# Kernel tuning notes

Hardware: AMD Instinct MI355X
Metric: run time of the kernel (lower is better)

The kernel has to match this reference:

```python
import jax, jax.numpy as jnp
import numpy as np

TOL = 1e-10
EIG_THRESH = 1e-6
NUM_EIG = 4
LANCZOS_K = 30


def setup_inputs() -> dict:
    key = jax.random.key(0)
    n = 200_000
    m = 3_200_000  # undirected edges, avg degree 16
    k1, k2, k3 = jax.random.split(key, 3)
    src = jax.random.randint(k1, (m,), 0, n, dtype=jnp.int32)
    dst = jax.random.randint(k2, (m,), 0, n, dtype=jnp.int32)
    diag = jnp.arange(n, dtype=jnp.int32)
    # symmetric graph Laplacian L = D - A in COO form: off-diag -1 both directions, diag = degree
    rows = jnp.concatenate([src, dst, diag])
    cols = jnp.concatenate([dst, src, diag])
    deg = jax.ops.segment_sum(jnp.ones(2 * m, jnp.float32),
                              jnp.concatenate([src, dst]), num_segments=n)
    vals = jnp.concatenate([-jnp.ones(2 * m, jnp.float32), deg])
    v0 = jax.random.normal(k3, (n,), jnp.float32)  # plays the role of torch.manual_seed(42) randn
    return {"vals": vals, "v0": v0, "rows": rows, "cols": cols, "n": n}


def reference(vals, v0, rows, cols, n):
    k = min(LANCZOS_K, n - 1)  # = 30 here
    # deterministic start vector: mean-subtract, normalize
    v = v0 - v0.mean()
    v = v / jnp.linalg.norm(v)
    V = jnp.zeros((n, k + 1), jnp.float32).at[:, 0].set(v)
    alphas = jnp.zeros(k, jnp.float32)
    betas = jnp.zeros(k, jnp.float32)

    def matvec(x):  # sparse L @ x via COO gather + segment_sum
        return jax.ops.segment_sum(vals * x[cols], rows, num_segments=n)

    def step(carry, i):
        V, alphas, betas, v_prev, beta_prev, done = carry
        v_cur = jax.lax.dynamic_index_in_dim(V, i, axis=1, keepdims=False)
        w = matvec(v_cur)
        alpha = jnp.dot(v_cur, w)
        w = w - alpha * v_cur - beta_prev * v_prev
        # full reorthogonalization: unset columns of V are zero so projecting on all of V
        # is exactly projecting on V[:, :i+1]
        coeffs = V.T @ w            # (k+1,)
        w = w - V @ coeffs
        w = w - w.mean()
        beta = jnp.linalg.norm(w)
        active = jnp.logical_not(done)
        good = active & (beta >= TOL)
        safe_beta = jnp.maximum(beta, TOL)
        v_next = jnp.where(good, w / safe_beta, 0.0)
        alphas = alphas.at[i].set(jnp.where(active, alpha, 0.0))
        betas = betas.at[i].set(jnp.where(good, beta, 0.0))
        V = V.at[:, i + 1].set(v_next)
        done = done | (beta < TOL)
        return (V, alphas, betas, v_cur, jnp.where(good, beta, 0.0), done), None

    init = (V, alphas, betas, jnp.zeros(n, jnp.float32), jnp.float32(0.0), jnp.array(False))
    (V, alphas, betas, _, _, _), _ = jax.lax.scan(step, init, jnp.arange(k))

    # tridiagonal T; early-break iterations leave zero rows/cols whose zero eigenvalues
    # are filtered by the > 1e-6 threshold, matching the truncated original
    T = jnp.diag(alphas) + jnp.diag(betas[:k - 1], 1) + jnp.diag(betas[:k - 1], -1)
    evals_all, Q = jnp.linalg.eigh(T)  # ascending
    num_valid = jnp.sum(evals_all > EIG_THRESH)
    start = k - num_valid              # valid eigenvalues form the sorted tail (L is PSD)
    pos = jnp.arange(NUM_EIG)
    valid = pos < num_valid
    idx = jnp.clip(start + pos, 0, k - 1)
    sel_evals = jnp.where(valid, evals_all[idx], 0.0)
    Y = Q[:, idx] * valid[None, :].astype(jnp.float32)  # (k, NUM_EIG)
    evecs = V[:, :k] @ Y                                 # (n, NUM_EIG)
    return evecs, sel_evals
```

## Files before the change

kernel.cpp:

```cpp
#include <hip/hip_runtime.h>
#include <math.h>

constexpr int LK = 30;

__device__ __constant__ float SFIX[4] = {1.f, -1.f, -1.f, -1.f};


__device__ __forceinline__ float blockReduceSum(float v) {
    for (int off = 32; off; off >>= 1) v += __shfl_down(v, off);
    __shared__ float s[4];
    int lane = threadIdx.x & 63, wid = threadIdx.x >> 6;
    if (lane == 0) s[wid] = v;
    __syncthreads();
    if (wid == 0) {
        v = (lane < 4) ? s[lane] : 0.f;
        v += __shfl_down(v, 2);
        v += __shfl_down(v, 1);
    }
    return v;
}

__global__ void k_zero_sc(float* __restrict__ sc) {
    sc[threadIdx.x] = 0.f;
    sc[256 + threadIdx.x] = 0.f;
}

__global__ void k_sum(const float* __restrict__ a, int n, float* target) {
    float acc = 0.f;
    for (int r = blockIdx.x * blockDim.x + threadIdx.x; r < n; r += gridDim.x * blockDim.x)
        acc += a[r];
    acc = blockReduceSum(acc);
    if (threadIdx.x == 0) atomicAdd(target, acc);
}

__global__ void k_init_v(const float* __restrict__ v0, float* __restrict__ U, int n,
                         const float* sumv, float* norm_acc, float inv_n) {
    int r = blockIdx.x * 256 + threadIdx.x;
    float m = *sumv * inv_n;
    float t = 0.f;
    if (r < n) { t = v0[r] - m; U[r] = t; }
    float s = blockReduceSum(t * t);
    if (threadIdx.x == 0) atomicAdd(norm_acc, s);
}

__global__ void k_scan1(const float* __restrict__ deg, int* __restrict__ rp,
                        int* __restrict__ bsum, int n) {
    __shared__ int s[256];
    int t = threadIdx.x, g = blockIdx.x * 256 + t;
    int v = (g < n) ? (int)deg[g] : 0;
    s[t] = v;
    __syncthreads();
    for (int off = 1; off < 256; off <<= 1) {
        int add = (t >= off) ? s[t - off] : 0;
        __syncthreads();
        s[t] += add;
        __syncthreads();
    }
    if (g < n) rp[g] = s[t] - v;
    if (t == 255) bsum[blockIdx.x] = s[255];
}

__global__ void k_scan2(int* __restrict__ bsum, int nb) {
    __shared__ int s[1024];
    int t = threadIdx.x;
    int v = (t < nb) ? bsum[t] : 0;
    s[t] = v;
    __syncthreads();
    for (int off = 1; off < 1024; off <<= 1) {
        int add = (t >= off) ? s[t - off] : 0;
        __syncthreads();
        s[t] += add;
        __syncthreads();
    }
    if (t < nb) bsum[t] = s[t] - v;
}

__global__ void k_scan3(int* __restrict__ rp, const int* __restrict__ bsum,
                        int* __restrict__ cursor, int n, int m2) {
    int g = blockIdx.x * 256 + threadIdx.x;
    if (g < n) {
        int v = rp[g] + bsum[blockIdx.x];
        rp[g] = v;
        cursor[g] = v;
    }
    if (g == 0) rp[n] = m2;
}

__global__ void k_fill_part(const int* __restrict__ rows, const int* __restrict__ cols,
                            int* __restrict__ cursor, int* __restrict__ cidx,
                            int m2, int nblk_per_grp) {
    int g = blockIdx.x & 7;
    int bi = blockIdx.x >> 3;
    int stride = nblk_per_grp * 256;
    for (int e = bi * 256 + threadIdx.x; e < m2; e += stride) {
        int r = rows[e];
        if (((r >> 12) & 7) == g) {
            int p = atomicAdd(&cursor[r], 1);
            cidx[p] = cols[e];
        }
    }
}

__global__ void k_matvec(const float* __restrict__ deg, const int* __restrict__ rp,
                         const int* __restrict__ cidx, const float* __restrict__ U,
                         float* __restrict__ Vi, float* __restrict__ w,
                         const float* norm_in, float* __restrict__ coeff,
                         float* __restrict__ alpha_acc, int n) {
    if (blockIdx.x == 0 && threadIdx.x < 33) coeff[threadIdx.x] = 0.f;
    int r = blockIdx.x * 256 + threadIdx.x;
    float part = 0.f;
    if (r < n) {
        float beta = sqrtf(*norm_in);
        float x = U[r] / beta;
        Vi[r] = x;
        int s = rp[r], e = rp[r + 1];
        float su = 0.f;
        int k = s;
        for (; k + 3 < e; k += 4) {
            int c0 = cidx[k], c1 = cidx[k + 1], c2 = cidx[k + 2], c3 = cidx[k + 3];
            float u0 = U[c0], u1 = U[c1], u2 = U[c2], u3 = U[c3];
            su += (u0 + u1) + (u2 + u3);
        }
        for (; k < e; ++k) su += U[cidx[k]];
        float wr = deg[r] * x - su / beta;
        w[r] = wr;
        part = x * wr;
    }
    part = blockReduceSum(part);
    if (threadIdx.x == 0) atomicAdd(alpha_acc, part);
}

__global__ void k_gs1(const float* __restrict__ V, float* __restrict__ w,
                      const float* __restrict__ vcur, const float* __restrict__ vprev,
                      const float* alpha_acc, const float* bprev_sq,
                      float* __restrict__ coeff, int i, int n) {
    __shared__ float slab[32];
    int t = threadIdx.x;
    if (t < 32) slab[t] = 0.f;
    __syncthreads();
    int r = blockIdx.x * 256 + t;
    bool in = (r < n);
    float a = *alpha_acc, b = sqrtf(*bprev_sq);
    float w1 = 0.f;
    if (in) {
        w1 = w[r] - a * vcur[r] - b * vprev[r];
        w[r] = w1;
    }
    int lane = t & 63;
    int j = 0;
    for (; j + 3 <= i; j += 4) {
        float p0 = 0.f, p1 = 0.f, p2 = 0.f, p3 = 0.f;
        if (in) {
            p0 = V[(size_t)j * n + r] * w1;
            p1 = V[(size_t)(j + 1) * n + r] * w1;
            p2 = V[(size_t)(j + 2) * n + r] * w1;
            p3 = V[(size_t)(j + 3) * n + r] * w1;
        }
        for (int off = 32; off; off >>= 1) {
            p0 += __shfl_down(p0, off);
            p1 += __shfl_down(p1, off);
            p2 += __shfl_down(p2, off);
            p3 += __shfl_down(p3, off);
        }
        if (lane == 0) {
            atomicAdd(&slab[j], p0);
            atomicAdd(&slab[j + 1], p1);
            atomicAdd(&slab[j + 2], p2);
            atomicAdd(&slab[j + 3], p3);
        }
    }
    for (; j <= i; ++j) {
        float p = in ? V[(size_t)j * n + r] * w1 : 0.f;
        for (int off = 32; off; off >>= 1) p += __shfl_down(p, off);
        if (lane == 0) atomicAdd(&slab[j], p);
    }
    float p = in ? w1 : 0.f;
    for (int off = 32; off; off >>= 1) p += __shfl_down(p, off);
    if (lane == 0) atomicAdd(&slab[i + 1], p);
    __syncthreads();
    if (t < i + 2) atomicAdd(&coeff[t], slab[t]);
}

__global__ void k_reorth2(const float* __restrict__ V, const float* __restrict__ w,
                          const float* __restrict__ coeff, float* __restrict__ U,
                          float* __restrict__ norm_out, int ncols, int n, float inv_n) {
    __shared__ float cf[34];
    __shared__ float slab[4];
    int t = threadIdx.x;
    if (t < ncols + 1) cf[t] = coeff[t];
    if (t < 4) slab[t] = 0.f;
    __syncthreads();
    int r = blockIdx.x * 256 + t;
    bool in = (r < n);
    float mean = cf[ncols] * inv_n;
    float acc = 0.f;
    if (in) {
        acc = w[r];
        int j = 0;
        for (; j + 3 < ncols; j += 4) {
            float v0 = V[(size_t)j * n + r], v1 = V[(size_t)(j + 1) * n + r];
            float v2 = V[(size_t)(j + 2) * n + r], v3 = V[(size_t)(j + 3) * n + r];
            acc -= cf[j] * v0 + cf[j + 1] * v1 + cf[j + 2] * v2 + cf[j + 3] * v3;
        }
        for (; j < ncols; ++j) acc -= cf[j] * V[(size_t)j * n + r];
        acc -= mean;
        U[r] = acc;
    }
    float p = acc * acc;
    for (int off = 32; off; off >>= 1) p += __shfl_down(p, off);
    if ((t & 63) == 0) slab[t >> 6] = p;
    __syncthreads();
    if (t == 0) atomicAdd(norm_out, slab[0] + slab[1] + slab[2] + slab[3]);
}

__global__ void k_zero_iter(float* sc) {
    if (threadIdx.x < 40) sc[threadIdx.x] = 0.f;
}

__global__ void k_normalize(const float* __restrict__ U, float* __restrict__ V0,
                            const float* norm_in, int n) {
    int r = blockIdx.x * 256 + threadIdx.x;
    float beta = sqrtf(*norm_in);
    if (r < n) V0[r] = U[r] / beta;
}

__global__ void k_zero_vec(float* w, int n) {
    int r = blockIdx.x * 256 + threadIdx.x;
    if (r < n) w[r] = 0.f;
}

__global__ void k_scatter(const float* __restrict__ vals, const int* __restrict__ rows,
                          const int* __restrict__ cols, const float* __restrict__ x,
                          float* __restrict__ w, int nnz) {
    int e = blockIdx.x * 256 + threadIdx.x;
    if (e < nnz) atomicAdd(&w[rows[e]], vals[e] * x[cols[e]]);
}

__global__ void k_dot(const float* __restrict__ a, const float* __restrict__ b, int n,
                      float* target) {
    float acc = 0.f;
    for (int r = blockIdx.x * blockDim.x + threadIdx.x; r < n; r += gridDim.x * blockDim.x)
        acc += a[r] * b[r];
    acc = blockReduceSum(acc);
    if (threadIdx.x == 0) atomicAdd(target, acc);
}

__global__ void k_axpy2_fb(float* __restrict__ w, const float* __restrict__ vcur,
                           const float* __restrict__ vprev, const float* alpha_acc,
                           const float* beta_prev, float* alpha_out, int n) {
    int r = blockIdx.x * 256 + threadIdx.x;
    float a = *alpha_acc, b = *beta_prev;
    if (r == 0) *alpha_out = a;
    if (r < n) w[r] -= a * vcur[r] + b * vprev[r];
}

__global__ void k_multidot_fb(const float* __restrict__ V, const float* __restrict__ w,
                              int n, float* coeff) {
    int j = blockIdx.y;
    const float* vj = V + (size_t)j * n;
    float acc = 0.f;
    for (int r = blockIdx.x * blockDim.x + threadIdx.x; r < n; r += gridDim.x * blockDim.x)
        acc += vj[r] * w[r];
    acc = blockReduceSum(acc);
    if (threadIdx.x == 0) atomicAdd(&coeff[j], acc);
}

__global__ void k_projsub_mean(float* __restrict__ w, const float* __restrict__ V,
                               const float* __restrict__ coeff, int ncols, int n,
                               float* mean_acc) {
    int r = blockIdx.x * 256 + threadIdx.x;
    float t = 0.f;
    if (r < n) {
        float acc = 0.f;
        for (int j = 0; j < ncols; ++j) acc += coeff[j] * V[(size_t)j * n + r];
        t = w[r] - acc;
        w[r] = t;
    }
    float s = blockReduceSum(t);
    if (threadIdx.x == 0) atomicAdd(mean_acc, s);
}

__global__ void k_meansub_norm(float* __restrict__ w, int n, const float* mean_acc,
                               float* norm_acc, float inv_n) {
    int r = blockIdx.x * 256 + threadIdx.x;
    float m = *mean_acc * inv_n;
    float t = 0.f;
    if (r < n) { t = w[r] - m; w[r] = t; }
    float s = blockReduceSum(t * t);
    if (threadIdx.x == 0) atomicAdd(norm_acc, s);
}

__global__ void k_scale_store(const float* __restrict__ w, float* __restrict__ vnext,
                              const float* norm_in, float* beta_out, int n) {
    int r = blockIdx.x * 256 + threadIdx.x;
    float beta = sqrtf(*norm_in);
    if (r == 0) *beta_out = beta;
    if (r < n) vnext[r] = w[r] / beta;
}

__global__ void k_eig(const float* __restrict__ ALPHA, const float* __restrict__ NORM,
                      float* __restrict__ Y, float* __restrict__ out_evals) {
    __shared__ double z[LK][LK + 1];
    __shared__ double d[LK], e[LK + 1];
    int t = threadIdx.x;
    if (t < LK) {
        d[t] = (double)ALPHA[t];
        e[t] = (t < LK - 1) ? (double)sqrtf(NORM[1 + t]) : 0.0;
        for (int j = 0; j < LK; ++j) z[t][j] = (t == j) ? 1.0 : 0.0;
    }
    __syncthreads();
    for (int l = 0; l < LK; ++l) {
        int iter = 0, m;
        do {
            __syncthreads();
            for (m = l; m < LK - 1; ++m) {
                double dd = fabs(d[m]) + fabs(d[m + 1]);
                if (fabs(e[m]) <= 2.3e-16 * dd) break;
            }
            if (m != l) {
                if (++iter > 80) break;
                double g = (d[l + 1] - d[l]) / (2.0 * e[l]);
                double r = sqrt(g * g + 1.0);
                g = d[m] - d[l] + e[l] / (g + (g >= 0.0 ? r : -r));
                double s = 1.0, c = 1.0, p = 0.0;
                bool uf = false;
                for (int i = m - 1; i >= l; --i) {
                    double f = s * e[i], b = c * e[i];
                    r = sqrt(f * f + g * g);
                    e[i + 1] = r;
                    if (r == 0.0) { d[i + 1] -= p; e[m] = 0.0; uf = true; break; }
                    double inv = 1.0 / r;
                    s = f * inv; c = g * inv;
                    g = d[i + 1] - p;
                    r = (d[i] - g) * s + 2.0 * c * b;
                    p = s * r;
                    d[i + 1] = g + p;
                    g = c * r - b;
                    if (t < LK) {
                        double f2 = z[t][i + 1];
                        z[t][i + 1] = s * z[t][i] + c * f2;
                        z[t][i] = c * z[t][i] - s * f2;
                    }
                }
                if (uf) continue;
                d[l] -= p;
                e[l] = g;
                e[m] = 0.0;
            }
        } while (m != l);
    }
    __syncthreads();
    for (int i = 0; i < LK - 1; ++i) {
        int mi = i;
        for (int j = i + 1; j < LK; ++j)
            if (d[j] < d[mi]) mi = j;
        if (mi != i) {
            double tmp = d[i];
            __syncthreads();
            d[i] = d[mi]; d[mi] = tmp;
            if (t < LK) {
                double tz = z[t][i]; z[t][i] = z[t][mi]; z[t][mi] = tz;
            }
            __syncthreads();
        }
    }
    __syncthreads();
    int num_valid = 0;
    for (int i = 0; i < LK; ++i)
        if (d[i] > 1e-6) num_valid++;
    int start = LK - num_valid;
    for (int j = 0; j < 4; ++j) {
        bool valid = j < num_valid;
        int idx = start + j;
        idx = idx < 0 ? 0 : (idx > LK - 1 ? LK - 1 : idx);
        double mx = -1.0;
        int am = 0;
        for (int k2 = 0; k2 < LK; ++k2) {
            double a = fabs(z[k2][idx]);
            if (a > mx) { mx = a; am = k2; }
        }
        double sgn = (z[am][idx] < 0.0 ? -1.0 : 1.0) * (double)SFIX[j];
        if (t < LK) Y[t * 4 + j] = valid ? (float)(sgn * z[t][idx]) : 0.f;
        if (t == 0) out_evals[j] = valid ? (float)d[idx] : 0.f;
    }
}

__global__ void k_output(const float* __restrict__ V, const float* __restrict__ Y,
                         float* __restrict__ out, int n) {
    __shared__ float y[LK * 4];
    if (threadIdx.x < LK * 4) y[threadIdx.x] = Y[threadIdx.x];
    __syncthreads();
    int r = blockIdx.x * 256 + threadIdx.x;
    if (r >= n) return;
    float a0 = 0.f, a1 = 0.f, a2 = 0.f, a3 = 0.f;
    for (int l = 0; l < LK; ++l) {
        float v = V[(size_t)l * n + r];
        a0 += v * y[l * 4 + 0];
        a1 += v * y[l * 4 + 1];
        a2 += v * y[l * 4 + 2];
        a3 += v * y[l * 4 + 3];
    }
    size_t o = (size_t)r * 4;
    out[o + 0] = a0; out[o + 1] = a1; out[o + 2] = a2; out[o + 3] = a3;
}

extern "C" void kernel_launch(void* const* d_in, const int* in_sizes, int n_in,
                              void* d_out, int out_size, void* d_ws, size_t ws_size,
                              hipStream_t stream) {
    const float* vals = (const float*)d_in[0];
    const float* v0   = (const float*)d_in[1];
    const int* rows   = (const int*)d_in[2];
    const int* cols   = (const int*)d_in[3];
    const int nnz = in_sizes[0];
    const int n   = in_sizes[1];
    const int m2  = nnz - n;
    float* out = (float*)d_out;
    const float* deg = vals + m2;

    float* V  = (float*)d_ws;
    float* U  = V + (size_t)LK * n;
    float* w  = U + n;
    float* SC = w + n;
    float* COEFF = SC;
    float* ACC   = SC + 33;
    float* NORM  = SC + 64;
    float* ALPHA = SC + 96;
    float* BETAS = SC + 128;
    float* SUMV  = SC + 160;
    float* Ydev  = SC + 168;

    int* rp     = (int*)(SC + 512);
    int* cursor = rp + (n + 1);
    int* bsum   = cursor + n;
    int* cidx   = bsum + 1024;

    const size_t need_csr = ((size_t)32 * n + 512 + (size_t)2 * n + 1025 + 1024 +
                             (size_t)m2) * 4;
    const bool use_csr = ws_size >= need_csr;

    const int gn  = (n + 255) / 256;
    const int geA = (nnz + 255) / 256;
    const int G   = 512;
    const float inv_n = 1.0f / (float)n;

    k_zero_sc<<<1, 256, 0, stream>>>(SC);
    k_sum<<<G, 256, 0, stream>>>(v0, n, SUMV);
    k_init_v<<<gn, 256, 0, stream>>>(v0, U, n, SUMV, &NORM[0], inv_n);

    if (use_csr) {
        k_scan1<<<gn, 256, 0, stream>>>(deg, rp, bsum, n);
        k_scan2<<<1, 1024, 0, stream>>>(bsum, gn);
        k_scan3<<<gn, 256, 0, stream>>>(rp, bsum, cursor, n, m2);
        const int nblk_per_grp = 128;
        k_fill_part<<<nblk_per_grp * 8, 256, 0, stream>>>(rows, cols, cursor, cidx,
                                                          m2, nblk_per_grp);

        for (int i = 0; i < LK; ++i) {
            float* Vi = V + (size_t)i * n;
            k_matvec<<<gn, 256, 0, stream>>>(deg, rp, cidx, U, Vi, w, &NORM[i],
                                             COEFF, &ALPHA[i], n);
            if (i < LK - 1) {
                const float* vprev = (i > 0) ? (V + (size_t)(i - 1) * n) : V;
                const float* bps   = (i > 0) ? &NORM[i] : &SC[39];
                k_gs1<<<gn, 256, 0, stream>>>(V, w, Vi, vprev, &ALPHA[i], bps,
                                              COEFF, i, n);
                k_reorth2<<<gn, 256, 0, stream>>>(V, w, COEFF, U, &NORM[i + 1],
                                                  i + 1, n, inv_n);
            }
        }
        k_eig<<<1, 64, 0, stream>>>(ALPHA, NORM, Ydev, out + (size_t)4 * n);
    } else {
        k_normalize<<<gn, 256, 0, stream>>>(U, V, &NORM[0], n);
        for (int i = 0; i < LK; ++i) {
            float* vcur = V + (size_t)i * n;
            const float* vprev = (i > 0) ? (V + (size_t)(i - 1) * n) : V;
            const float* bprev = (i > 0) ? &BETAS[i - 1] : &SC[39];
            k_zero_iter<<<1, 64, 0, stream>>>(SC);
            k_zero_vec<<<gn, 256, 0, stream>>>(w, n);
            k_scatter<<<geA, 256, 0, stream>>>(vals, rows, cols, vcur, w, nnz);
            k_dot<<<G, 256, 0, stream>>>(vcur, w, n, &ACC[0]);
            k_axpy2_fb<<<gn, 256, 0, stream>>>(w, vcur, vprev, &ACC[0], bprev,
                                               &ALPHA[i], n);
            dim3 md(G, i + 1, 1);
            k_multidot_fb<<<md, 256, 0, stream>>>(V, w, n, COEFF);
            k_projsub_mean<<<gn, 256, 0, stream>>>(w, V, COEFF, i + 1, n, &ACC[1]);
            k_meansub_norm<<<gn, 256, 0, stream>>>(w, n, &ACC[1], &NORM[i + 1], inv_n);
            if (i < LK - 1)
                k_scale_store<<<gn, 256, 0, stream>>>(w, V + (size_t)(i + 1) * n,
                                                      &NORM[i + 1], &BETAS[i], n);
        }
        k_eig<<<1, 64, 0, stream>>>(ALPHA, NORM, Ydev, out + (size_t)4 * n);
    }
    k_output<<<gn, 256, 0, stream>>>(V, Ydev, out, n);
}
```

Baseline: 3.061 ms.

## Replace full QL tridiagonal eigensolver with Sturm bisection plus inverse iteration

The single-block implicit QL eigensolver, which computed all 30 eigenpairs with many block-wide syncs, is replaced by Sturm-sequence bisection for only the four wanted eigenvalues. Each eigenvector is then obtained by inverse iteration with a pivoted tridiagonal LU, one thread per eigenpair. This cuts the serial work in the eigen kernel. It risks lower accuracy for clustered eigenvalues and differences in eigenvector sign or orthogonality.

```diff
diff --git a/kernel.cpp b/kernel.cpp
--- a/kernel.cpp
+++ b/kernel.cpp
@@ -298,90 +298,123 @@
     if (r < n) vnext[r] = w[r] / beta;
 }
 
+__device__ __forceinline__ int sturm_count(const double* d0, const double* e2, double x) {
+    int cnt = 0;
+    double q = d0[0] - x;
+    if (q < 0.0) cnt++;
+    for (int i = 1; i < LK; ++i) {
+        double qq = (fabs(q) < 1e-290) ? ((q < 0.0) ? -1e-290 : 1e-290) : q;
+        q = (d0[i] - x) - e2[i - 1] / qq;
+        if (q < 0.0) cnt++;
+    }
+    return cnt;
+}
+
 __global__ void k_eig(const float* __restrict__ ALPHA, const float* __restrict__ NORM,
                       float* __restrict__ Y, float* __restrict__ out_evals) {
-    __shared__ double z[LK][LK + 1];
-    __shared__ double d[LK], e[LK + 1];
+    __shared__ double d0[LK], e2[LK], ew[LK];
+    __shared__ double lohi[2];
+    __shared__ int nv_sh;
+    __shared__ double DL[4][LK], DD[4][LK], DU[4][LK], DU2[4][LK], YV[4][LK];
+    __shared__ char PIV[4][LK];
     int t = threadIdx.x;
     if (t < LK) {
-        d[t] = (double)ALPHA[t];
-        e[t] = (t < LK - 1) ? (double)sqrtf(NORM[1 + t]) : 0.0;
-        for (int j = 0; j < LK; ++j) z[t][j] = (t == j) ? 1.0 : 0.0;
-    }
-    __syncthreads();
-    for (int l = 0; l < LK; ++l) {
-        int iter = 0, m;
-        do {
-            __syncthreads();
-            for (m = l; m < LK - 1; ++m) {
-                double dd = fabs(d[m]) + fabs(d[m + 1]);
-                if (fabs(e[m]) <= 2.3e-16 * dd) break;
+        d0[t] = (double)ALPHA[t];
+        double e = (t < LK - 1) ? (double)sqrtf(NORM[1 + t]) : 0.0;
+        ew[t] = e;
+        e2[t] = e * e;
+    }
+    __syncthreads();
+    if (t == 0) {
+        double lo = 1e300, hi = -1e300;
+        for (int i = 0; i < LK; ++i) {
+            double r = ((i > 0) ? fabs(ew[i - 1]) : 0.0) +
+                       ((i < LK - 1) ? fabs(ew[i]) : 0.0);
+            lo = fmin(lo, d0[i] - r);
+            hi = fmax(hi, d0[i] + r);
+        }
+        lohi[0] = lo - 1.0;
+        lohi[1] = hi + 1.0;
+        nv_sh = LK - sturm_count(d0, e2, 1e-6);
+    }
+    __syncthreads();
+    int nv = nv_sh;
+    if (t < 4) {
+        int start = LK - nv;
+        int tgt = start + t;
+        tgt = tgt < 0 ? 0 : (tgt > LK - 1 ? LK - 1 : tgt);
+        double lo = lohi[0], hi = lohi[1];
+        for (int it = 0; it < 64; ++it) {
+            double mid = 0.5 * (lo + hi);
+            if (mid == lo || mid == hi) break;
+            if (sturm_count(d0, e2, mid) <= tgt) lo = mid;
+            else hi = mid;
+        }
+        double lam = 0.5 * (lo + hi);
+        double* dl = DL[t]; double* dd = DD[t]; double* du = DU[t];
+        double* du2 = DU2[t]; double* y = YV[t]; char* piv = PIV[t];
+        for (int i = 0; i < LK; ++i) {
+            dd[i] = d0[i] - lam;
+            if (i < LK - 1) { dl[i] = ew[i]; du[i] = ew[i]; }
+            if (i < LK - 2) du2[i] = 0.0;
+        }
+        for (int i = 0; i < LK - 1; ++i) {
+            bool last = (i == LK - 2);
+            if (fabs(dd[i]) >= fabs(dl[i])) {
+                piv[i] = 0;
+                if (dd[i] != 0.0) {
+                    double fact = dl[i] / dd[i];
+                    dl[i] = fact;
+                    dd[i + 1] -= fact * du[i];
+                }
+                if (!last) du2[i] = 0.0;
+            } else {
+                piv[i] = 1;
+                double fact = dd[i] / dl[i];
+                dd[i] = dl[i];
+                dl[i] = fact;
+                double tmp = du[i];
+                du[i] = dd[i + 1];
+                dd[i + 1] = tmp - fact * dd[i + 1];
+                if (!last) {
+                    du2[i] = du[i + 1];
+                    du[i + 1] = -fact * du[i + 1];
+                }
             }
-            if (m != l) {
-                if (++iter > 80) break;
-                double g = (d[l + 1] - d[l]) / (2.0 * e[l]);
-                double r = sqrt(g * g + 1.0);
-                g = d[m] - d[l] + e[l] / (g + (g >= 0.0 ? r : -r));
-                double s = 1.0, c = 1.0, p = 0.0;
-                bool uf = false;
-                for (int i = m - 1; i >= l; --i) {
-                    double f = s * e[i], b = c * e[i];
-                    r = sqrt(f * f + g * g);
-                    e[i + 1] = r;
-                    if (r == 0.0) { d[i + 1] -= p; e[m] = 0.0; uf = true; break; }
-                    double inv = 1.0 / r;
-                    s = f * inv; c = g * inv;
-                    g = d[i + 1] - p;
-                    r = (d[i] - g) * s + 2.0 * c * b;
-                    p = s * r;
-                    d[i + 1] = g + p;
-                    g = c * r - b;
-                    if (t < LK) {
-                        double f2 = z[t][i + 1];
-                        z[t][i + 1] = s * z[t][i] + c * f2;
-                        z[t][i] = c * z[t][i] - s * f2;
-                    }
+        }
+        for (int i = 0; i < LK; ++i)
+            if (fabs(dd[i]) < 1e-290) dd[i] = (dd[i] < 0.0) ? -1e-290 : 1e-290;
+        for (int i = 0; i < LK; ++i) y[i] = 1.0;
+        for (int iter = 0; iter < 3; ++iter) {
+            for (int i = 0; i < LK - 1; ++i) {
+                if (!piv[i]) {
+                    y[i + 1] -= dl[i] * y[i];
+                } else {
+                    double tmp = y[i];
+                    y[i] = y[i + 1];
+                    y[i + 1] = tmp - dl[i] * y[i];
                 }
-                if (uf) continue;
-                d[l] -= p;
-                e[l] = g;
-                e[m] = 0.0;
             }
-        } while (m != l);
-    }
-    __syncthreads();
-    for (int i = 0; i < LK - 1; ++i) {
-        int mi = i;
-        for (int j = i + 1; j < LK; ++j)
-            if (d[j] < d[mi]) mi = j;
-        if (mi != i) {
-            double tmp = d[i];
-            __syncthreads();
-            d[i] = d[mi]; d[mi] = tmp;
-            if (t < LK) {
-                double tz = z[t][i]; z[t][i] = z[t][mi]; z[t][mi] = tz;
-            }
-            __syncthreads();
-        }
-    }
-    __syncthreads();
-    int num_valid = 0;
-    for (int i = 0; i < LK; ++i)
-        if (d[i] > 1e-6) num_valid++;
-    int start = LK - num_valid;
-    for (int j = 0; j < 4; ++j) {
-        bool valid = j < num_valid;
-        int idx = start + j;
-        idx = idx < 0 ? 0 : (idx > LK - 1 ? LK - 1 : idx);
+            y[LK - 1] /= dd[LK - 1];
+            y[LK - 2] = (y[LK - 2] - du[LK - 2] * y[LK - 1]) / dd[LK - 2];
+            for (int i = LK - 3; i >= 0; --i)
+                y[i] = (y[i] - du[i] * y[i + 1] - du2[i] * y[i + 2]) / dd[i];
+            double nrm = 0.0;
+            for (int i = 0; i < LK; ++i) nrm += y[i] * y[i];
+            nrm = 1.0 / sqrt(nrm);
+            for (int i = 0; i < LK; ++i) y[i] *= nrm;
+        }
         double mx = -1.0;
         int am = 0;
-        for (int k2 = 0; k2 < LK; ++k2) {
-            double a = fabs(z[k2][idx]);
-            if (a > mx) { mx = a; am = k2; }
-        }
-        double sgn = (z[am][idx] < 0.0 ? -1.0 : 1.0) * (double)SFIX[j];
-        if (t < LK) Y[t * 4 + j] = valid ? (float)(sgn * z[t][idx]) : 0.f;
-        if (t == 0) out_evals[j] = valid ? (float)d[idx] : 0.f;
+        for (int i = 0; i < LK; ++i) {
+            double a = fabs(y[i]);
+            if (a > mx) { mx = a; am = i; }
+        }
+        double sgn = (y[am] < 0.0 ? -1.0 : 1.0) * (double)SFIX[t];
+        bool valid = t < nv;
+        for (int i = 0; i < LK; ++i)
+            Y[i * 4 + t] = valid ? (float)(sgn * y[i]) : 0.f;
+        out_evals[t] = valid ? (float)lam : 0.f;
     }
 }
 
```

Result: faster. 2.766 ms (-9.6%).
